# Kernel optimization log

Measured on AMD Instinct MI355X. Metric: run time of the kernel, lower is better.

## Reference

```python
import jax, jax.numpy as jnp
import numpy as np

B, C, H, W = 4, 256, 64, 64

def _conv1x1(x, Wt, b):
    # x: [b,c,h,w], Wt: [out,in], b: [out]
    return jnp.einsum('bchw,dc->bdhw', x, Wt) + b[None, :, None, None]

def setup_inputs() -> dict:
    key = jax.random.key(0)
    ks = jax.random.split(key, 10)
    s = 1.0 / np.sqrt(C)
    return {
        'F_c': jax.random.normal(ks[0], (B, C, H, W), jnp.float32),
        'F_s': jax.random.normal(ks[1], (B, C, H, W), jnp.float32),
        'Wf': jax.random.normal(ks[2], (C, C), jnp.float32) * s,
        'bf': jnp.zeros((C,), jnp.float32),
        'Wg': jax.random.normal(ks[3], (C, C), jnp.float32) * s,
        'bg': jnp.zeros((C,), jnp.float32),
        'Wh': jax.random.normal(ks[4], (C, C), jnp.float32) * s,
        'bh': jnp.zeros((C,), jnp.float32),
        'Wo': jax.random.normal(ks[5], (C, C), jnp.float32) * s,
        'bo': jnp.zeros((C,), jnp.float32),
    }

def reference(F_c, F_s, Wf, bf, Wg, bg, Wh, bh, Wo, bo):
    b, c, h, w = F_c.shape
    Fq = _conv1x1(F_c, Wf, bf).reshape(b, c, -1)          # [b,c,Nc]
    G = _conv1x1(F_s, Wg, bg).reshape(b, c, -1)           # [b,c,Ns]
    Hv = _conv1x1(F_s, Wh, bh).reshape(b, c, -1)          # [b,c,Ns]
    S = jnp.einsum('bcn,bcm->bnm', Fq, G)                 # [b,Nc,Ns] (unscaled)
    S = jax.nn.softmax(S, axis=-1)
    res = jnp.einsum('bcm,bnm->bcn', Hv, S)               # [b,c,Nc]
    res = res.reshape(b, c, h, w)
    return _conv1x1(res, Wo, bo)
```

## Files before the change

### kernel.cpp

```cpp
#include <hip/hip_runtime.h>
#include <stdint.h>

#define NB 4
#define CC 256
#define NN 4096
#define KITERS 32
#define WAIT_LGKM0 0xC07F

typedef __attribute__((ext_vector_type(8))) _Float16 half8;
typedef __attribute__((ext_vector_type(4))) _Float16 half4;
typedef __attribute__((ext_vector_type(2))) _Float16 half2v;
typedef __attribute__((ext_vector_type(4))) float floatx4;
typedef __attribute__((ext_vector_type(16))) float float16v;
typedef __attribute__((ext_vector_type(4))) int intx4;

__device__ __forceinline__ void cvt16v(float4 a, float4 b, float4 c, float4 d,
                                       half8& lo, half8& hi) {
  lo[0] = (_Float16)a.x; lo[1] = (_Float16)a.y; lo[2] = (_Float16)a.z; lo[3] = (_Float16)a.w;
  lo[4] = (_Float16)b.x; lo[5] = (_Float16)b.y; lo[6] = (_Float16)b.z; lo[7] = (_Float16)b.w;
  hi[0] = (_Float16)c.x; hi[1] = (_Float16)c.y; hi[2] = (_Float16)c.z; hi[3] = (_Float16)c.w;
  hi[4] = (_Float16)d.x; hi[5] = (_Float16)d.y; hi[6] = (_Float16)d.z; hi[7] = (_Float16)d.w;
}

__device__ __forceinline__ int packh2(float a, float b) {
  half2v p; p[0] = (_Float16)a; p[1] = (_Float16)b;
  return __builtin_bit_cast(int, p);
}

__device__ __forceinline__ void a16(const _Float16* g, _Float16* l) {
  __builtin_amdgcn_global_load_lds(
      (__attribute__((address_space(1))) void*)(uintptr_t)g,
      (__attribute__((address_space(3))) void*)l, 16, 0, 0);
}

__global__ __launch_bounds__(256, 3) void k_qkv(const float* __restrict__ Fc,
                                                const float* __restrict__ Fs,
                                                const float* __restrict__ Wf,
                                                const float* __restrict__ Wg,
                                                const float* __restrict__ Wh,
                                                const float* __restrict__ bf,
                                                const float* __restrict__ bg,
                                                const float* __restrict__ bh,
                                                _Float16* __restrict__ Qs,
                                                _Float16* __restrict__ Ks,
                                                _Float16* __restrict__ Vs) {
  __shared__ float tmp[32][132];
  __shared__ _Float16 As[128][40];
  __shared__ _Float16 Bs[128][40];
  const int z = blockIdx.z, bz = blockIdx.y;
  const float* F = ((z == 0) ? Fc : Fs) + (size_t)bz * CC * NN;
  const float* W = (z == 0) ? Wf : ((z == 1) ? Wg : Wh);
  const float* bias = (z == 0) ? bf : ((z == 1) ? bg : bh);
  int mt, nt;
  if (z < 2) { mt = blockIdx.x >> 5; nt = blockIdx.x & 31; }
  else       { mt = blockIdx.x >> 1; nt = blockIdx.x & 1;  }
  const int m0 = mt * 128, n0 = nt * 128;
  const int xn0 = (z < 2) ? n0 : m0;
  const int wd0 = (z < 2) ? m0 : n0;
  const int tid = threadIdx.x;
  const int wave = tid >> 6, lane = tid & 63, quad = lane >> 4, l15 = lane & 15;
  const int wm = (wave >> 1) * 64, wn = (wave & 1) * 64;

  floatx4 acc[4][4];
#pragma unroll
  for (int i = 0; i < 4; i++)
#pragma unroll
    for (int j = 0; j < 4; j++) acc[i][j] = (floatx4){0.f, 0.f, 0.f, 0.f};

  const int srow = tid >> 1, shalf = (tid & 1) * 16;
  const int fc = tid >> 3, fn = (tid & 7) * 16;
  const int xr = tid >> 1, xh = (tid & 1) * 16;

  float4 wr0, wr1, wr2, wr3, fr0, fr1, fr2, fr3;
  {
    const float4* wp = (const float4*)(W + (size_t)(wd0 + srow) * 256 + 0 + shalf);
    wr0 = wp[0]; wr1 = wp[1]; wr2 = wp[2]; wr3 = wp[3];
    const float4* fp = (const float4*)(F + (size_t)(0 + fc) * NN + xn0 + fn);
    fr0 = fp[0]; fr1 = fp[1]; fr2 = fp[2]; fr3 = fp[3];
  }

  for (int kk = 0; kk < 256; kk += 32) {
    __syncthreads();
    *(float4*)&tmp[fc][fn + 0] = fr0;
    *(float4*)&tmp[fc][fn + 4] = fr1;
    *(float4*)&tmp[fc][fn + 8] = fr2;
    *(float4*)&tmp[fc][fn + 12] = fr3;
    half8 w_lo, w_hi;
    cvt16v(wr0, wr1, wr2, wr3, w_lo, w_hi);
    if (z < 2) {
      *(half8*)&As[srow][shalf] = w_lo;
      *(half8*)&As[srow][shalf + 8] = w_hi;
    } else {
      *(half8*)&Bs[srow][shalf] = w_lo;
      *(half8*)&Bs[srow][shalf + 8] = w_hi;
    }
    __syncthreads();
    if (kk + 32 < 256) {
      const float4* wp = (const float4*)(W + (size_t)(wd0 + srow) * 256 + kk + 32 + shalf);
      wr0 = wp[0]; wr1 = wp[1]; wr2 = wp[2]; wr3 = wp[3];
      const float4* fp = (const float4*)(F + (size_t)(kk + 32 + fc) * NN + xn0 + fn);
      fr0 = fp[0]; fr1 = fp[1]; fr2 = fp[2]; fr3 = fp[3];
    }
    half8 xlo, xhi;
#pragma unroll
    for (int i = 0; i < 8; i++) xlo[i] = (_Float16)tmp[xh + i][xr];
#pragma unroll
    for (int i = 0; i < 8; i++) xhi[i] = (_Float16)tmp[xh + 8 + i][xr];
    if (z < 2) {
      *(half8*)&Bs[xr][xh] = xlo;
      *(half8*)&Bs[xr][xh + 8] = xhi;
    } else {
      *(half8*)&As[xr][xh] = xlo;
      *(half8*)&As[xr][xh + 8] = xhi;
    }
    __syncthreads();
    half8 af[4], bfr[4];
#pragma unroll
    for (int mb = 0; mb < 4; mb++) af[mb] = *(const half8*)&As[wm + mb * 16 + l15][quad * 8];
#pragma unroll
    for (int nb = 0; nb < 4; nb++) bfr[nb] = *(const half8*)&Bs[wn + nb * 16 + l15][quad * 8];
#pragma unroll
    for (int mb = 0; mb < 4; mb++)
#pragma unroll
      for (int nb = 0; nb < 4; nb++)
        acc[mb][nb] = __builtin_amdgcn_mfma_f32_16x16x32_f16(af[mb], bfr[nb], acc[mb][nb], 0, 0, 0);
  }

  if (z < 2) {
    _Float16* op = (z == 0 ? Qs : Ks) + (size_t)bz * NN * CC;
#pragma unroll
    for (int mb = 0; mb < 4; mb++) {
      int d0 = m0 + wm + mb * 16 + quad * 4;
      float b0 = bias[d0], b1 = bias[d0 + 1], b2 = bias[d0 + 2], b3 = bias[d0 + 3];
      const int cs = d0 >> 4, hh = (d0 >> 3) & 1, j0 = d0 & 7;
#pragma unroll
      for (int nb = 0; nb < 4; nb++) {
        int n_ = n0 + wn + nb * 16 + l15;
        int kt = n_ >> 5, ql_ = n_ & 31;
        half4 pk;
        pk[0] = (_Float16)(acc[mb][nb][0] + b0);
        pk[1] = (_Float16)(acc[mb][nb][1] + b1);
        pk[2] = (_Float16)(acc[mb][nb][2] + b2);
        pk[3] = (_Float16)(acc[mb][nb][3] + b3);
        size_t idx = ((size_t)(kt * 16 + cs) * 64 + ql_ + 32 * hh) * 8 + j0;
        *(half4*)(op + idx) = pk;
      }
    }
  } else {
    _Float16* op = Vs + (size_t)bz * NN * CC;
#pragma unroll
    for (int mb = 0; mb < 4; mb++) {
      int nq0 = m0 + wm + mb * 16 + quad * 4;
      const int kt = nq0 >> 5, krel = nq0 & 31;
      const int hk = krel >> 4, hh = (krel >> 3) & 1, j0 = krel & 7;
#pragma unroll
      for (int nb = 0; nb < 4; nb++) {
        int d = n0 + wn + nb * 16 + l15;
        int ql_ = d & 31, g = (d >> 5) & 7;
        float bv = bias[d];
        half4 pk;
        pk[0] = (_Float16)(acc[mb][nb][0] + bv);
        pk[1] = (_Float16)(acc[mb][nb][1] + bv);
        pk[2] = (_Float16)(acc[mb][nb][2] + bv);
        pk[3] = (_Float16)(acc[mb][nb][3] + bv);
        size_t idx = (((size_t)(kt * 8 + g) * 2 + hk) * 64 + ql_ + 32 * hh) * 8 + j0;
        *(half4*)(op + idx) = pk;
      }
    }
  }
}

__global__ __launch_bounds__(256, 2) void k_attn(const _Float16* __restrict__ Q,
                                                 const _Float16* __restrict__ K,
                                                 const _Float16* __restrict__ Vt,
                                                 _Float16* __restrict__ Opart,
                                                 float2* __restrict__ Ml) {
  __shared__ _Float16 smem[8192 * 4];
  const int tid = threadIdx.x;
  const int wave = tid >> 6, lane = tid & 63;

  const int qt = blockIdx.x, ck = blockIdx.y, b = blockIdx.z;
  const int ql = lane & 31, h = lane >> 5;
  const int q0 = qt * 128 + wave * 32;
  const _Float16* Qb = Q + (size_t)b * NN * CC;
  const _Float16* Kg = K + (size_t)b * NN * CC;
  const _Float16* Vg = Vt + (size_t)b * NN * CC;
  const int kt_base = ck * KITERS;
  const int so = wave * 512;
  const int go = wave * 512 + lane * 8;

  const int ktq = q0 >> 5;
  half8 qf[16];
#pragma unroll
  for (int cs = 0; cs < 16; cs++)
    qf[cs] = *(const half8*)(Qb + ((size_t)(ktq * 16 + cs) * 64 + lane) * 8);

  float16v Oa[8];
#pragma unroll
  for (int g = 0; g < 8; g++)
#pragma unroll
    for (int i = 0; i < 16; i++) Oa[g][i] = 0.f;

  float m_run = -1e30f, l_run = 0.f;
  half8 pf0, pf1;
#pragma unroll
  for (int i = 0; i < 8; i++) { pf0[i] = (_Float16)0.f; pf1[i] = (_Float16)0.f; }

  {
    const _Float16* Kt = Kg + (size_t)kt_base * 8192;
#pragma unroll
    for (int p = 0; p < 4; p++) a16(Kt + p * 2048 + go, smem + p * 2048 + so);
  }

  for (int t = 0; t < KITERS; t++) {
    asm volatile("s_waitcnt vmcnt(0)" ::: "memory");
    __builtin_amdgcn_s_barrier();
    {
      const _Float16* Vtile = Vg + (size_t)(kt_base + t) * 8192;
      _Float16* Vw = smem + (2 + (t & 1)) * 8192;
#pragma unroll
      for (int p = 0; p < 4; p++) a16(Vtile + p * 2048 + go, Vw + p * 2048 + so);
      if (t + 1 < KITERS) {
        const _Float16* Kt = Kg + (size_t)(kt_base + t + 1) * 8192;
        _Float16* Kw = smem + ((t + 1) & 1) * 8192;
#pragma unroll
        for (int p = 0; p < 4; p++) a16(Kt + p * 2048 + go, Kw + p * 2048 + so);
      }
    }
    const _Float16* Kl = smem + (t & 1) * 8192;

    float16v s, s2;
#pragma unroll
    for (int i = 0; i < 16; i++) { s[i] = 0.f; s2[i] = 0.f; }
    __builtin_amdgcn_s_setprio(1);
    if (t > 0) {
      const _Float16* Vr = smem + (2 + ((t - 1) & 1)) * 8192;
#pragma unroll
      for (int i = 0; i < 16; i++) {
        half8 kf = *(const half8*)(Kl + i * 512 + lane * 8);
        if (i & 1)
          s2 = __builtin_amdgcn_mfma_f32_32x32x16_f16(kf, qf[i], s2, 0, 0, 0);
        else
          s = __builtin_amdgcn_mfma_f32_32x32x16_f16(kf, qf[i], s, 0, 0, 0);
        const int u = i & 7, ks = i >> 3;
        half8 vf = *(const half8*)(Vr + (2 * u + ks) * 512 + lane * 8);
        Oa[u] = __builtin_amdgcn_mfma_f32_32x32x16_f16(vf, ks ? pf1 : pf0, Oa[u], 0, 0, 0);
      }
    } else {
#pragma unroll
      for (int cs = 0; cs < 16; cs += 2) {
        half8 kfa = *(const half8*)(Kl + cs * 512 + lane * 8);
        s = __builtin_amdgcn_mfma_f32_32x32x16_f16(kfa, qf[cs], s, 0, 0, 0);
        half8 kfb = *(const half8*)(Kl + (cs + 1) * 512 + lane * 8);
        s2 = __builtin_amdgcn_mfma_f32_32x32x16_f16(kfb, qf[cs + 1], s2, 0, 0, 0);
      }
    }
    __builtin_amdgcn_s_setprio(0);
#pragma unroll
    for (int i = 0; i < 16; i++) s[i] += s2[i];

    float t0 = fmaxf(s[0], s[1]), t1 = fmaxf(s[2], s[3]);
    float t2 = fmaxf(s[4], s[5]), t3 = fmaxf(s[6], s[7]);
    float t4 = fmaxf(s[8], s[9]), t5 = fmaxf(s[10], s[11]);
    float t6 = fmaxf(s[12], s[13]), t7 = fmaxf(s[14], s[15]);
    t0 = fmaxf(t0, t1); t2 = fmaxf(t2, t3); t4 = fmaxf(t4, t5); t6 = fmaxf(t6, t7);
    float tmax = fmaxf(fmaxf(t0, t2), fmaxf(t4, t6));
    tmax = fmaxf(tmax, __shfl_xor(tmax, 32));
    bool need = tmax > m_run + 8.0f;
    if (__any((int)need)) {
      float mN = need ? tmax : m_run;
      float alpha = __expf(m_run - mN);
      m_run = mN;
      l_run *= alpha;
#pragma unroll
      for (int g = 0; g < 8; g++)
#pragma unroll
        for (int i = 0; i < 16; i++) Oa[g][i] *= alpha;
    }
#pragma unroll
    for (int i = 0; i < 16; i++) s[i] = __expf(s[i] - m_run);
    float u0 = (s[0] + s[1]) + (s[2] + s[3]);
    float u1 = (s[4] + s[5]) + (s[6] + s[7]);
    float u2 = (s[8] + s[9]) + (s[10] + s[11]);
    float u3 = (s[12] + s[13]) + (s[14] + s[15]);
    float ts = (u0 + u1) + (u2 + u3);
    ts += __shfl_xor(ts, 32);
    l_run += ts;

    {
      int A01 = packh2(s[0], s[1]), B23 = packh2(s[2], s[3]);
      int C45 = packh2(s[4], s[5]), D67 = packh2(s[6], s[7]);
      int E01 = packh2(s[8], s[9]), F23 = packh2(s[10], s[11]);
      int G45 = packh2(s[12], s[13]), H67 = packh2(s[14], s[15]);
      auto rA = __builtin_amdgcn_permlane32_swap(A01, C45, false, false);
      auto rB = __builtin_amdgcn_permlane32_swap(B23, D67, false, false);
      auto rC = __builtin_amdgcn_permlane32_swap(E01, G45, false, false);
      auto rD = __builtin_amdgcn_permlane32_swap(F23, H67, false, false);
      intx4 w0, w1;
      w0[0] = rA[0]; w0[1] = rB[0]; w0[2] = rA[1]; w0[3] = rB[1];
      w1[0] = rC[0]; w1[1] = rD[0]; w1[2] = rC[1]; w1[3] = rD[1];
      pf0 = __builtin_bit_cast(half8, w0);
      pf1 = __builtin_bit_cast(half8, w1);
    }
  }

  asm volatile("s_waitcnt vmcnt(0)" ::: "memory");
  __builtin_amdgcn_s_barrier();
  {
    const _Float16* Vr = smem + (2 + ((KITERS - 1) & 1)) * 8192;
#pragma unroll
    for (int u = 0; u < 8; u++) {
      half8 vfa = *(const half8*)(Vr + (2 * u) * 512 + lane * 8);
      Oa[u] = __builtin_amdgcn_mfma_f32_32x32x16_f16(vfa, pf0, Oa[u], 0, 0, 0);
    }
#pragma unroll
    for (int u = 0; u < 8; u++) {
      half8 vfb = *(const half8*)(Vr + (2 * u + 1) * 512 + lane * 8);
      Oa[u] = __builtin_amdgcn_mfma_f32_32x32x16_f16(vfb, pf1, Oa[u], 0, 0, 0);
    }
  }

  float invl = 1.f / l_run;
  __syncthreads();
  float* ot = (float*)smem + wave * (32 * 33);
  _Float16* Opb = Opart + ((size_t)ck * NB + b) * NN * CC;
  const int qr = lane >> 1;
  const int chalf = (lane & 1) * 16;
#pragma unroll
  for (int g = 0; g < 8; g++) {
#pragma unroll
    for (int r = 0; r < 16; r++)
      ot[((r & 3) + 8 * (r >> 2) + 4 * h) * 33 + ql] = Oa[g][r] * invl;
    __builtin_amdgcn_s_waitcnt(WAIT_LGKM0);
    half8 o0, o1;
#pragma unroll
    for (int i = 0; i < 8; i++) o0[i] = (_Float16)ot[(chalf + i) * 33 + qr];
#pragma unroll
    for (int i = 0; i < 8; i++) o1[i] = (_Float16)ot[(chalf + 8 + i) * 33 + qr];
    _Float16* gp = Opb + (size_t)(q0 + qr) * CC + g * 32 + chalf;
    *(half8*)gp = o0;
    *(half8*)(gp + 8) = o1;
    __builtin_amdgcn_s_waitcnt(WAIT_LGKM0);
  }
  if (h == 0) {
    float2 ml; ml.x = m_run; ml.y = l_run;
    Ml[((size_t)ck * NB + b) * NN + q0 + ql] = ml;
  }
}

__global__ __launch_bounds__(256, 2) void k_out(const _Float16* __restrict__ Opart,
                                                const float2* __restrict__ Ml,
                                                const float* __restrict__ Wo,
                                                const float* __restrict__ bo,
                                                float* __restrict__ out) {
  __shared__ _Float16 As[64][72];
  __shared__ _Float16 Bs[128][72];
  const int bz = blockIdx.y;
  const int mt = blockIdx.x >> 1, nt = blockIdx.x & 1;
  const int m0 = mt * 64, n0 = nt * 128;
  const int tid = threadIdx.x;
  const int wave = tid >> 6, lane = tid & 63, quad = lane >> 4, l15 = lane & 15;
  const int wn = wave * 32;

  floatx4 acc[4][2];
#pragma unroll
  for (int i = 0; i < 4; i++)
#pragma unroll
    for (int j = 0; j < 2; j++) acc[i][j] = (floatx4){0.f, 0.f, 0.f, 0.f};

  const int arow = tid >> 2, acol = (tid & 3) * 16;
  const int brow = tid >> 1, bcol = (tid & 1) * 32;

  const size_t qi = (size_t)bz * NN + m0 + arow;
  float2 a0 = Ml[qi], a1 = Ml[(size_t)NB * NN + qi];
  float2 a2 = Ml[(size_t)2 * NB * NN + qi], a3 = Ml[(size_t)3 * NB * NN + qi];
  float M = fmaxf(fmaxf(a0.x, a1.x), fmaxf(a2.x, a3.x));
  float w0 = __expf(a0.x - M) * a0.y, w1 = __expf(a1.x - M) * a1.y;
  float w2 = __expf(a2.x - M) * a2.y, w3 = __expf(a3.x - M) * a3.y;
  float inv = 1.f / (w0 + w1 + w2 + w3);
  w0 *= inv; w1 *= inv; w2 *= inv; w3 *= inv;
  const size_t ps = (size_t)NB * NN * CC;
  const _Float16* prow = Opart + qi * CC;

  half8 pA[4][2];
  float4 wr[8];
  {
    const _Float16* pr = prow + acol;
#pragma unroll
    for (int pl = 0; pl < 4; pl++) {
      pA[pl][0] = *(const half8*)(pr + (size_t)pl * ps);
      pA[pl][1] = *(const half8*)(pr + (size_t)pl * ps + 8);
    }
    const float4* wp = (const float4*)(Wo + (size_t)(n0 + brow) * 256 + bcol);
#pragma unroll
    for (int i = 0; i < 8; i++) wr[i] = wp[i];
  }

  for (int kk = 0; kk < 256; kk += 64) {
    half8 ma0, ma1;
#pragma unroll
    for (int i = 0; i < 8; i++) {
      ma0[i] = (_Float16)(w0 * (float)pA[0][0][i] + w1 * (float)pA[1][0][i] +
                          w2 * (float)pA[2][0][i] + w3 * (float)pA[3][0][i]);
      ma1[i] = (_Float16)(w0 * (float)pA[0][1][i] + w1 * (float)pA[1][1][i] +
                          w2 * (float)pA[2][1][i] + w3 * (float)pA[3][1][i]);
    }
    half8 bl0, bh0, bl1, bh1;
    cvt16v(wr[0], wr[1], wr[2], wr[3], bl0, bh0);
    cvt16v(wr[4], wr[5], wr[6], wr[7], bl1, bh1);
    __syncthreads();
    *(half8*)&As[arow][acol] = ma0;
    *(half8*)&As[arow][acol + 8] = ma1;
    *(half8*)&Bs[brow][bcol] = bl0;
    *(half8*)&Bs[brow][bcol + 8] = bh0;
    *(half8*)&Bs[brow][bcol + 16] = bl1;
    *(half8*)&Bs[brow][bcol + 24] = bh1;
    __syncthreads();
    if (kk + 64 < 256) {
      const _Float16* pr = prow + kk + 64 + acol;
#pragma unroll
      for (int pl = 0; pl < 4; pl++) {
        pA[pl][0] = *(const half8*)(pr + (size_t)pl * ps);
        pA[pl][1] = *(const half8*)(pr + (size_t)pl * ps + 8);
      }
      const float4* wp = (const float4*)(Wo + (size_t)(n0 + brow) * 256 + kk + 64 + bcol);
#pragma unroll
      for (int i = 0; i < 8; i++) wr[i] = wp[i];
    }
#pragma unroll
    for (int ks = 0; ks < 2; ks++) {
      half8 af[4], bfr[2];
#pragma unroll
      for (int mb = 0; mb < 4; mb++)
        af[mb] = *(const half8*)&As[mb * 16 + l15][ks * 32 + quad * 8];
#pragma unroll
      for (int nb = 0; nb < 2; nb++)
        bfr[nb] = *(const half8*)&Bs[wn + nb * 16 + l15][ks * 32 + quad * 8];
#pragma unroll
      for (int mb = 0; mb < 4; mb++)
#pragma unroll
        for (int nb = 0; nb < 2; nb++)
          acc[mb][nb] = __builtin_amdgcn_mfma_f32_16x16x32_f16(af[mb], bfr[nb], acc[mb][nb], 0, 0, 0);
    }
  }

  float* op = out + (size_t)bz * NN * CC;
#pragma unroll
  for (int mb = 0; mb < 4; mb++) {
    int nq0 = m0 + mb * 16 + quad * 4;
#pragma unroll
    for (int nb = 0; nb < 2; nb++) {
      int d = n0 + wn + nb * 16 + l15;
      float bv = bo[d];
      floatx4 pk;
      pk[0] = acc[mb][nb][0] + bv;
      pk[1] = acc[mb][nb][1] + bv;
      pk[2] = acc[mb][nb][2] + bv;
      pk[3] = acc[mb][nb][3] + bv;
      *(floatx4*)(op + (size_t)d * NN + nq0) = pk;
    }
  }
}

extern "C" void kernel_launch(void* const* d_in, const int* in_sizes, int n_in,
                              void* d_out, int out_size, void* d_ws, size_t ws_size,
                              hipStream_t stream) {
  const float* Fc = (const float*)d_in[0];
  const float* Fs = (const float*)d_in[1];
  const float* Wf = (const float*)d_in[2];
  const float* bf_ = (const float*)d_in[3];
  const float* Wg = (const float*)d_in[4];
  const float* bg = (const float*)d_in[5];
  const float* Wh = (const float*)d_in[6];
  const float* bh = (const float*)d_in[7];
  const float* Wo = (const float*)d_in[8];
  const float* bo = (const float*)d_in[9];

  char* ws = (char*)d_ws;
  const size_t sz = (size_t)NB * NN * CC * sizeof(_Float16);
  _Float16* Opart = (_Float16*)(ws + 0 * sz);
  _Float16* Qs = (_Float16*)(ws + 4 * sz);
  _Float16* Ks = (_Float16*)(ws + 5 * sz);
  _Float16* Vs = (_Float16*)(ws + 6 * sz);
  float2* Ml = (float2*)(ws + 7 * sz);

  k_qkv<<<dim3(64, NB, 3), 256, 0, stream>>>(Fc, Fs, Wf, Wg, Wh, bf_, bg, bh, Qs, Ks, Vs);
  k_attn<<<dim3(32, 4, NB), 256, 0, stream>>>(Qs, Ks, Vs, Opart, Ml);
  k_out<<<dim3(128, NB), 256, 0, stream>>>(Opart, Ml, Wo, bo, (float*)d_out);
}
```

Measured before the change: 195.9 us.

## Fuse K and V projections into one kernel pass sharing the F_s tile

```diff
diff --git a/kernel.cpp b/kernel.cpp
--- a/kernel.cpp
+++ b/kernel.cpp
@@ -33,7 +33,7 @@
       (__attribute__((address_space(3))) void*)l, 16, 0, 0);
 }
 
-__global__ __launch_bounds__(256, 3) void k_qkv(const float* __restrict__ Fc,
+__global__ __launch_bounds__(256, 2) void k_qkv(const float* __restrict__ Fc,
                                                 const float* __restrict__ Fs,
                                                 const float* __restrict__ Wf,
                                                 const float* __restrict__ Wg,
@@ -45,36 +45,41 @@
                                                 _Float16* __restrict__ Ks,
                                                 _Float16* __restrict__ Vs) {
   __shared__ float tmp[32][132];
-  __shared__ _Float16 As[128][40];
-  __shared__ _Float16 Bs[128][40];
+  __shared__ _Float16 Gs[128][40];
+  __shared__ _Float16 Hs[128][40];
+  __shared__ _Float16 Xs[128][40];
   const int z = blockIdx.z, bz = blockIdx.y;
   const float* F = ((z == 0) ? Fc : Fs) + (size_t)bz * CC * NN;
-  const float* W = (z == 0) ? Wf : ((z == 1) ? Wg : Wh);
-  const float* bias = (z == 0) ? bf : ((z == 1) ? bg : bh);
-  int mt, nt;
-  if (z < 2) { mt = blockIdx.x >> 5; nt = blockIdx.x & 31; }
-  else       { mt = blockIdx.x >> 1; nt = blockIdx.x & 1;  }
-  const int m0 = mt * 128, n0 = nt * 128;
-  const int xn0 = (z < 2) ? n0 : m0;
-  const int wd0 = (z < 2) ? m0 : n0;
+  const float* W1 = (z == 0) ? Wf : Wg;
+  const int dblk = blockIdx.x >> 5, nblk = blockIdx.x & 31;
+  const int wd0 = dblk * 128;
+  const int xn0 = nblk * 128;
   const int tid = threadIdx.x;
   const int wave = tid >> 6, lane = tid & 63, quad = lane >> 4, l15 = lane & 15;
   const int wm = (wave >> 1) * 64, wn = (wave & 1) * 64;
 
-  floatx4 acc[4][4];
+  floatx4 acck[4][4];
+  floatx4 accv[4][4];
 #pragma unroll
   for (int i = 0; i < 4; i++)
 #pragma unroll
-    for (int j = 0; j < 4; j++) acc[i][j] = (floatx4){0.f, 0.f, 0.f, 0.f};
+    for (int j = 0; j < 4; j++) {
+      acck[i][j] = (floatx4){0.f, 0.f, 0.f, 0.f};
+      accv[i][j] = (floatx4){0.f, 0.f, 0.f, 0.f};
+    }
 
   const int srow = tid >> 1, shalf = (tid & 1) * 16;
   const int fc = tid >> 3, fn = (tid & 7) * 16;
   const int xr = tid >> 1, xh = (tid & 1) * 16;
 
-  float4 wr0, wr1, wr2, wr3, fr0, fr1, fr2, fr3;
+  float4 wg0, wg1, wg2, wg3, wh0, wh1, wh2, wh3, fr0, fr1, fr2, fr3;
   {
-    const float4* wp = (const float4*)(W + (size_t)(wd0 + srow) * 256 + 0 + shalf);
-    wr0 = wp[0]; wr1 = wp[1]; wr2 = wp[2]; wr3 = wp[3];
+    const float4* wp = (const float4*)(W1 + (size_t)(wd0 + srow) * 256 + 0 + shalf);
+    wg0 = wp[0]; wg1 = wp[1]; wg2 = wp[2]; wg3 = wp[3];
+    if (z) {
+      const float4* hp = (const float4*)(Wh + (size_t)(wd0 + srow) * 256 + 0 + shalf);
+      wh0 = hp[0]; wh1 = hp[1]; wh2 = hp[2]; wh3 = hp[3];
+    }
     const float4* fp = (const float4*)(F + (size_t)(0 + fc) * NN + xn0 + fn);
     fr0 = fp[0]; fr1 = fp[1]; fr2 = fp[2]; fr3 = fp[3];
   }
@@ -85,19 +90,26 @@
     *(float4*)&tmp[fc][fn + 4] = fr1;
     *(float4*)&tmp[fc][fn + 8] = fr2;
     *(float4*)&tmp[fc][fn + 12] = fr3;
-    half8 w_lo, w_hi;
-    cvt16v(wr0, wr1, wr2, wr3, w_lo, w_hi);
-    if (z < 2) {
-      *(half8*)&As[srow][shalf] = w_lo;
-      *(half8*)&As[srow][shalf + 8] = w_hi;
-    } else {
-      *(half8*)&Bs[srow][shalf] = w_lo;
-      *(half8*)&Bs[srow][shalf + 8] = w_hi;
+    {
+      half8 w_lo, w_hi;
+      cvt16v(wg0, wg1, wg2, wg3, w_lo, w_hi);
+      *(half8*)&Gs[srow][shalf] = w_lo;
+      *(half8*)&Gs[srow][shalf + 8] = w_hi;
+      if (z) {
+        half8 h_lo, h_hi;
+        cvt16v(wh0, wh1, wh2, wh3, h_lo, h_hi);
+        *(half8*)&Hs[srow][shalf] = h_lo;
+        *(half8*)&Hs[srow][shalf + 8] = h_hi;
+      }
     }
     __syncthreads();
     if (kk + 32 < 256) {
-      const float4* wp = (const float4*)(W + (size_t)(wd0 + srow) * 256 + kk + 32 + shalf);
-      wr0 = wp[0]; wr1 = wp[1]; wr2 = wp[2]; wr3 = wp[3];
+      const float4* wp = (const float4*)(W1 + (size_t)(wd0 + srow) * 256 + kk + 32 + shalf);
+      wg0 = wp[0]; wg1 = wp[1]; wg2 = wp[2]; wg3 = wp[3];
+      if (z) {
+        const float4* hp = (const float4*)(Wh + (size_t)(wd0 + srow) * 256 + kk + 32 + shalf);
+        wh0 = hp[0]; wh1 = hp[1]; wh2 = hp[2]; wh3 = hp[3];
+      }
       const float4* fp = (const float4*)(F + (size_t)(kk + 32 + fc) * NN + xn0 + fn);
       fr0 = fp[0]; fr1 = fp[1]; fr2 = fp[2]; fr3 = fp[3];
     }
@@ -106,63 +118,74 @@
     for (int i = 0; i < 8; i++) xlo[i] = (_Float16)tmp[xh + i][xr];
 #pragma unroll
     for (int i = 0; i < 8; i++) xhi[i] = (_Float16)tmp[xh + 8 + i][xr];
-    if (z < 2) {
-      *(half8*)&Bs[xr][xh] = xlo;
-      *(half8*)&Bs[xr][xh + 8] = xhi;
-    } else {
-      *(half8*)&As[xr][xh] = xlo;
-      *(half8*)&As[xr][xh + 8] = xhi;
-    }
+    *(half8*)&Xs[xr][xh] = xlo;
+    *(half8*)&Xs[xr][xh + 8] = xhi;
     __syncthreads();
-    half8 af[4], bfr[4];
-#pragma unroll
-    for (int mb = 0; mb < 4; mb++) af[mb] = *(const half8*)&As[wm + mb * 16 + l15][quad * 8];
-#pragma unroll
-    for (int nb = 0; nb < 4; nb++) bfr[nb] = *(const half8*)&Bs[wn + nb * 16 + l15][quad * 8];
-#pragma unroll
-    for (int mb = 0; mb < 4; mb++)
-#pragma unroll
-      for (int nb = 0; nb < 4; nb++)
-        acc[mb][nb] = __builtin_amdgcn_mfma_f32_16x16x32_f16(af[mb], bfr[nb], acc[mb][nb], 0, 0, 0);
-  }
-
-  if (z < 2) {
+    {
+      half8 af[4], bfr[4];
+#pragma unroll
+      for (int mb = 0; mb < 4; mb++) af[mb] = *(const half8*)&Gs[wm + mb * 16 + l15][quad * 8];
+#pragma unroll
+      for (int nb = 0; nb < 4; nb++) bfr[nb] = *(const half8*)&Xs[wn + nb * 16 + l15][quad * 8];
+#pragma unroll
+      for (int mb = 0; mb < 4; mb++)
+#pragma unroll
+        for (int nb = 0; nb < 4; nb++)
+          acck[mb][nb] = __builtin_amdgcn_mfma_f32_16x16x32_f16(af[mb], bfr[nb], acck[mb][nb], 0, 0, 0);
+    }
+    if (z) {
+      half8 av[4], bv[4];
+#pragma unroll
+      for (int mb = 0; mb < 4; mb++) av[mb] = *(const half8*)&Xs[wm + mb * 16 + l15][quad * 8];
+#pragma unroll
+      for (int nb = 0; nb < 4; nb++) bv[nb] = *(const half8*)&Hs[wn + nb * 16 + l15][quad * 8];
+#pragma unroll
+      for (int mb = 0; mb < 4; mb++)
+#pragma unroll
+        for (int nb = 0; nb < 4; nb++)
+          accv[mb][nb] = __builtin_amdgcn_mfma_f32_16x16x32_f16(av[mb], bv[nb], accv[mb][nb], 0, 0, 0);
+    }
+  }
+
+  {
+    const float* bias = (z == 0) ? bf : bg;
     _Float16* op = (z == 0 ? Qs : Ks) + (size_t)bz * NN * CC;
 #pragma unroll
     for (int mb = 0; mb < 4; mb++) {
-      int d0 = m0 + wm + mb * 16 + quad * 4;
+      int d0 = wd0 + wm + mb * 16 + quad * 4;
       float b0 = bias[d0], b1 = bias[d0 + 1], b2 = bias[d0 + 2], b3 = bias[d0 + 3];
       const int cs = d0 >> 4, hh = (d0 >> 3) & 1, j0 = d0 & 7;
 #pragma unroll
       for (int nb = 0; nb < 4; nb++) {
-        int n_ = n0 + wn + nb * 16 + l15;
+        int n_ = xn0 + wn + nb * 16 + l15;
         int kt = n_ >> 5, ql_ = n_ & 31;
         half4 pk;
-        pk[0] = (_Float16)(acc[mb][nb][0] + b0);
-        pk[1] = (_Float16)(acc[mb][nb][1] + b1);
-        pk[2] = (_Float16)(acc[mb][nb][2] + b2);
-        pk[3] = (_Float16)(acc[mb][nb][3] + b3);
+        pk[0] = (_Float16)(acck[mb][nb][0] + b0);
+        pk[1] = (_Float16)(acck[mb][nb][1] + b1);
+        pk[2] = (_Float16)(acck[mb][nb][2] + b2);
+        pk[3] = (_Float16)(acck[mb][nb][3] + b3);
         size_t idx = ((size_t)(kt * 16 + cs) * 64 + ql_ + 32 * hh) * 8 + j0;
         *(half4*)(op + idx) = pk;
       }
     }
-  } else {
+  }
+  if (z) {
     _Float16* op = Vs + (size_t)bz * NN * CC;
 #pragma unroll
     for (int mb = 0; mb < 4; mb++) {
-      int nq0 = m0 + wm + mb * 16 + quad * 4;
+      int nq0 = xn0 + wm + mb * 16 + quad * 4;
       const int kt = nq0 >> 5, krel = nq0 & 31;
       const int hk = krel >> 4, hh = (krel >> 3) & 1, j0 = krel & 7;
 #pragma unroll
       for (int nb = 0; nb < 4; nb++) {
-        int d = n0 + wn + nb * 16 + l15;
+        int d = wd0 + wn + nb * 16 + l15;
         int ql_ = d & 31, g = (d >> 5) & 7;
-        float bv = bias[d];
+        float bv2 = bh[d];
         half4 pk;
-        pk[0] = (_Float16)(acc[mb][nb][0] + bv);
-        pk[1] = (_Float16)(acc[mb][nb][1] + bv);
-        pk[2] = (_Float16)(acc[mb][nb][2] + bv);
-        pk[3] = (_Float16)(acc[mb][nb][3] + bv);
+        pk[0] = (_Float16)(accv[mb][nb][0] + bv2);
+        pk[1] = (_Float16)(accv[mb][nb][1] + bv2);
+        pk[2] = (_Float16)(accv[mb][nb][2] + bv2);
+        pk[3] = (_Float16)(accv[mb][nb][3] + bv2);
         size_t idx = (((size_t)(kt * 8 + g) * 2 + hk) * 64 + ql_ + 32 * hh) * 8 + j0;
         *(half4*)(op + idx) = pk;
       }
@@ -484,7 +507,7 @@
   _Float16* Vs = (_Float16*)(ws + 6 * sz);
   float2* Ml = (float2*)(ws + 7 * sz);
 
-  k_qkv<<<dim3(64, NB, 3), 256, 0, stream>>>(Fc, Fs, Wf, Wg, Wh, bf_, bg, bh, Qs, Ks, Vs);
+  k_qkv<<<dim3(64, NB, 2), 256, 0, stream>>>(Fc, Fs, Wf, Wg, Wh, bf_, bg, bh, Qs, Ks, Vs);
   k_attn<<<dim3(32, 4, NB), 256, 0, stream>>>(Qs, Ks, Vs, Opart, Ml);
   k_out<<<dim3(128, NB), 256, 0, stream>>>(Opart, Ml, Wo, bo, (float*)d_out);
 }
```

Result: slower. 200.2 us (+2.2%).
